# Kernel tuning notes

Measured on AMD Instinct MI355X. Metric: run time of the kernel, lower is better.

Reference implementation:

```python
import jax, jax.numpy as jnp
import numpy as np
import math

NEG_INF = -10000.0

def setup_inputs() -> dict:
    key = jax.random.key(0)
    k1, k2, k3 = jax.random.split(key, 3)
    B, Sq, Sk, H, D = 2, 2048, 2048, 16, 64
    q = jax.random.normal(k1, (B, Sq, H, D), dtype=jnp.float32)
    kv = jax.random.normal(k2, (B, Sk, 2, H, D), dtype=jnp.float32)
    key_padding_mask = jax.random.randint(k3, (B, Sk), 0, 2).astype(jnp.bool_)
    return {"q": q, "kv": kv, "key_padding_mask": key_padding_mask}

def reference(q, kv, key_padding_mask):
    # q: (B, Sq, H, D); kv: (B, Sk, 2, H, D); key_padding_mask: (B, Sk) True=keep
    D = q.shape[-1]
    softmax_scale = 1.0 / math.sqrt(D)
    k = kv[:, :, 0]  # (B, Sk, H, D)
    v = kv[:, :, 1]  # (B, Sk, H, D)
    # (B, H, Sq, Sk) score matrix
    scores = jnp.einsum('bthd,bshd->bhts', q, k * softmax_scale)
    # additive padding mask: 0 where keep, NEG_INF where masked out
    pad = jnp.where(key_padding_mask, 0.0, NEG_INF).astype(scores.dtype)
    scores = scores + pad[:, None, None, :]
    attention = jax.nn.softmax(scores, axis=-1)
    # dropout_p = 0.0 (eval mode) -> no-op
    output = jnp.einsum('bhts,bshd->bthd', attention, v)
    return output
```

## Files before the change

kernel.cpp:

```cpp
#include <hip/hip_runtime.h>

typedef unsigned short u16;
typedef unsigned int   u32;
typedef u16   u16x8 __attribute__((ext_vector_type(8)));
typedef float f32x4 __attribute__((ext_vector_type(4)));
typedef __bf16 bf16x8 __attribute__((ext_vector_type(8)));
typedef u32   u32x2 __attribute__((ext_vector_type(2)));
typedef u32   u32x4 __attribute__((ext_vector_type(4)));

#define QSCALE  0.18033688011112f
#define BM_OPEN  -28.8539008177793f
#define BM_MASK  -14455.8043097f

__device__ __forceinline__ u16 f2bf(float x){
  __bf16 h = (__bf16)x;
  return __builtin_bit_cast(u16, h);
}
__device__ __forceinline__ f32x4 mfma16x16x32(u16x8 a, u16x8 b, f32x4 c){
  return __builtin_amdgcn_mfma_f32_16x16x32_bf16(
      __builtin_bit_cast(bf16x8, a), __builtin_bit_cast(bf16x8, b), c, 0, 0, 0);
}
__device__ __forceinline__ void gld16(const void* g, void* l){
  __builtin_amdgcn_global_load_lds(
      (const __attribute__((address_space(1))) u32*)g,
      (__attribute__((address_space(3))) u32*)l, 16, 0, 0);
}


__global__ __launch_bounds__(256, 4)
void prepass(const float* __restrict__ KV, const int* __restrict__ MASK,
             u16* __restrict__ IMG, float* __restrict__ BIASM)
{
  const int tid = threadIdx.x;
  const int bid = blockIdx.x;
  const int kt = bid & 31;
  const int h  = (bid >> 5) & 15;
  const int b  = bid >> 9;
  const int kb = kt*64;
  const size_t kv_b = (size_t)b*(2048u*2048u);
  u16* tile = IMG + (size_t)bid * 8192;

  {
    const int skey = tid >> 2, scp = tid & 3;
    const float* kp = KV + kv_b + (size_t)(kb + skey)*2048 + h*64 + 16*scp;
    f32x4 f0 = *(const f32x4*)(kp);
    f32x4 f1 = *(const f32x4*)(kp + 4);
    f32x4 f2 = *(const f32x4*)(kp + 8);
    f32x4 f3 = *(const f32x4*)(kp + 12);
    u16x8 c0, c1;
    #pragma unroll
    for (int e = 0; e < 4; ++e){
      c0[e] = f2bf(f0[e]); c0[e+4] = f2bf(f1[e]);
      c1[e] = f2bf(f2[e]); c1[e+4] = f2bf(f3[e]);
    }
    const int idx0 = skey*64 + (((2*scp) ^ (skey & 7)) << 3);
    *(u16x8*)&tile[idx0]     = c0;
    *(u16x8*)&tile[idx0 ^ 8] = c1;
  }
  {
    const int sdb = tid & 7, ssp = tid >> 3;
    const float* vp = KV + kv_b + (size_t)(kb + 2*ssp)*2048 + 1024 + h*64 + 8*sdb;
    f32x4 r0a = *(const f32x4*)(vp);
    f32x4 r0b = *(const f32x4*)(vp + 4);
    f32x4 r1a = *(const f32x4*)(vp + 2048);
    f32x4 r1b = *(const f32x4*)(vp + 2048 + 4);
    u32* vimg = (u32*)(tile + 4096);
    const int wc = ssp >> 2, wi = ssp & 3;
    #pragma unroll
    for (int j = 0; j < 4; ++j){
      const int d0 = 8*sdb + j;
      const int d1 = d0 + 4;
      vimg[d0*32 + ((wc ^ (d0 & 7)) << 2) + wi] = (u32)f2bf(r0a[j]) | ((u32)f2bf(r1a[j]) << 16);
      vimg[d1*32 + ((wc ^ (d1 & 7)) << 2) + wi] = (u32)f2bf(r0b[j]) | ((u32)f2bf(r1b[j]) << 16);
    }
  }
  if (h == 0 && tid < 64){
    const int s = kb + tid;
    BIASM[b*2048 + s] = MASK[b*2048 + s] ? BM_OPEN : BM_MASK;
  }
}

template<int PRE>
__global__ __launch_bounds__(256, 2)
void attn_main(const float* __restrict__ Q, const float* __restrict__ KV,
               const int* __restrict__ MASK, const u16* __restrict__ IMG,
               const float* __restrict__ BIASM, float* __restrict__ OUT)
{
  __shared__ __align__(16) u16 KVbuf[3][8192];
  __shared__ __align__(16) u32 Pw[4][32*36];

  const int tid  = threadIdx.x;
  const int w    = tid >> 6;
  const int lane = tid & 63;
  const int lg   = lane >> 4;
  const int ln   = lane & 15;

  const int bid0 = blockIdx.x;
  const int bid  = (bid0 & 7)*64 + (bid0 >> 3);
  const int qt  = bid & 15;
  const int h   = (bid >> 4) & 15;
  const int b   = bid >> 8;

  const int qbase = qt*128 + w*32;
  const size_t q_b  = (size_t)b * (2048u*1024u);
  const size_t kv_b = (size_t)b * (2048u*2048u);

  const int lnoff = ln*64;
  const int ck0   = ((lg ^ (ln & 7)) << 3);
  const int ck1   = ck0 ^ 32;

  u16x8 Qf[2][2];
  #pragma unroll
  for (int G = 0; G < 2; ++G){
    const int qrow = qbase + 16*G + ln;
    const float* qp = Q + q_b + (size_t)qrow*1024 + h*64 + 8*lg;
    #pragma unroll
    for (int kc = 0; kc < 2; ++kc){
      f32x4 a = *(const f32x4*)(qp + 32*kc);
      f32x4 c = *(const f32x4*)(qp + 32*kc + 4);
      u16x8 v;
      #pragma unroll
      for (int e = 0; e < 4; ++e){
        v[e]     = f2bf(a[e] * QSCALE);
        v[e + 4] = f2bf(c[e] * QSCALE);
      }
      Qf[G][kc] = v;
    }
  }

  f32x4 Oacc[2][4];
  #pragma unroll
  for (int G = 0; G < 2; ++G)
    #pragma unroll
    for (int dt = 0; dt < 4; ++dt)
      Oacc[G][dt] = f32x4{0.f,0.f,0.f,0.f};
  float lrun[2] = { 0.f, 0.f };

  const char* img0 = (const char*)IMG + (size_t)((b*16 + h)*32) * 16384;
  const int so = tid*16;
  const int skey = tid >> 2, scp = tid & 3;
  const int sdb  = tid & 7,  ssp = tid >> 3;
  const float* kp0 = KV + kv_b + (size_t)skey*2048 + h*64 + 16*scp;
  const float* vp0 = KV + kv_b + (size_t)(2*ssp)*2048 + 1024 + h*64 + 8*sdb;
  f32x4 kf0, kf1, kf2, kf3, va, vb2, vc, vd;

#define STAGE_ISSUE(T, DST) do{                                               \
    const char* g_ = img0 + (size_t)(T)*16384;                                \
    char* l_ = (char*)(DST);                                                  \
    gld16(g_+so,        l_+so);                                               \
    gld16(g_+so+4096,   l_+so+4096);                                          \
    gld16(g_+so+8192,   l_+so+8192);                                          \
    gld16(g_+so+12288,  l_+so+12288);                                         \
  }while(0)

#define STAGE_REG(T) do{                                                      \
    const float* kp_ = kp0 + (size_t)(T)*64*2048;                             \
    kf0=*(const f32x4*)(kp_);   kf1=*(const f32x4*)(kp_+4);                   \
    kf2=*(const f32x4*)(kp_+8); kf3=*(const f32x4*)(kp_+12);                  \
    const float* vp_ = vp0 + (size_t)(T)*64*2048;                             \
    va=*(const f32x4*)(vp_);      vb2=*(const f32x4*)(vp_+4);                 \
    vc=*(const f32x4*)(vp_+2048); vd =*(const f32x4*)(vp_+2048+4);            \
  }while(0)

#define STAGE_WRITE(DST) do{                                                  \
    u16x8 c0_, c1_;                                                           \
    _Pragma("unroll") for (int e_=0; e_<4; ++e_){                             \
      c0_[e_]=f2bf(kf0[e_]); c0_[e_+4]=f2bf(kf1[e_]);                         \
      c1_[e_]=f2bf(kf2[e_]); c1_[e_+4]=f2bf(kf3[e_]); }                       \
    const int kix_ = skey*64 + (((2*scp) ^ (skey & 7)) << 3);                 \
    *(u16x8*)&(DST)[kix_]     = c0_;                                          \
    *(u16x8*)&(DST)[kix_ ^ 8] = c1_;                                          \
    u32* vimg_ = (u32*)((DST)+4096);                                          \
    const int wc_ = ssp >> 2, wi_ = ssp & 3;                                  \
    _Pragma("unroll") for (int j_=0; j_<4; ++j_){                             \
      const int d0_=8*sdb+j_, d1_=d0_+4;                                      \
      vimg_[d0_*32 + ((wc_ ^ (d0_&7)) << 2) + wi_] = (u32)f2bf(va[j_])  | ((u32)f2bf(vc[j_])<<16); \
      vimg_[d1_*32 + ((wc_ ^ (d1_&7)) << 2) + wi_] = (u32)f2bf(vb2[j_]) | ((u32)f2bf(vd[j_])<<16); \
    }                                                                         \
  }while(0)

#define COMPUTE(T, CUR) do{                                                   \
    const u16* Kb_ = (CUR);                                                   \
    const u16* Vb_ = (CUR) + 4096;                                            \
    f32x4 S[2][4];                                                            \
    _Pragma("unroll") for (int ct = 0; ct < 4; ++ct){                         \
      f32x4 bv;                                                               \
      if constexpr (PRE){                                                     \
        bv = *(const f32x4*)(BIASM + b*2048 + (T)*64 + 16*ct + 4*lg);         \
      } else {                                                                \
        const int4 mv = *(const int4*)(MASK + b*2048 + (T)*64 + 16*ct + 4*lg);\
        bv[0] = mv.x ? BM_OPEN : BM_MASK;                                     \
        bv[1] = mv.y ? BM_OPEN : BM_MASK;                                     \
        bv[2] = mv.z ? BM_OPEN : BM_MASK;                                     \
        bv[3] = mv.w ? BM_OPEN : BM_MASK;                                     \
      }                                                                       \
      S[0][ct] = bv;                                                          \
      S[1][ct] = bv;                                                          \
    }                                                                         \
    __builtin_amdgcn_s_setprio(1);                                            \
    _Pragma("unroll") for (int ct = 0; ct < 4; ++ct){                         \
      const int rb = ct*1024 + lnoff;                                         \
      u16x8 k0 = *(const u16x8*)&Kb_[rb + ck0];                               \
      u16x8 k1 = *(const u16x8*)&Kb_[rb + ck1];                               \
      S[0][ct] = mfma16x16x32(k0, Qf[0][0], S[0][ct]);                        \
      S[1][ct] = mfma16x16x32(k0, Qf[1][0], S[1][ct]);                        \
      S[0][ct] = mfma16x16x32(k1, Qf[0][1], S[0][ct]);                        \
      S[1][ct] = mfma16x16x32(k1, Qf[1][1], S[1][ct]);                        \
    }                                                                         \
    __builtin_amdgcn_s_setprio(0);                                            \
    _Pragma("unroll") for (int G = 0; G < 2; ++G){                            \
      float ps = 0.f;                                                         \
      _Pragma("unroll") for (int ct = 0; ct < 4; ++ct){                       \
        _Pragma("unroll") for (int r = 0; r < 4; ++r){                        \
          const float p = __builtin_amdgcn_exp2f(S[G][ct][r]);                \
          S[G][ct][r] = p;                                                    \
          ps += p;                                                            \
        }                                                                     \
      }                                                                       \
      lrun[G] += ps;                                                          \
      _Pragma("unroll") for (int ct = 0; ct < 4; ++ct){                       \
        u32x2 pw;                                                             \
        pw[0] = (u32)f2bf(S[G][ct][0]) | ((u32)f2bf(S[G][ct][1]) << 16);      \
        pw[1] = (u32)f2bf(S[G][ct][2]) | ((u32)f2bf(S[G][ct][3]) << 16);      \
        *(u32x2*)&Pw[w][(16*G + ln)*36 + 8*ct + 2*lg] = pw;                   \
      }                                                                       \
    }                                                                         \
    asm volatile("" ::: "memory");                                            \
    u16x8 Pf[2][2];                                                           \
    _Pragma("unroll") for (int G = 0; G < 2; ++G)                             \
      _Pragma("unroll") for (int sc = 0; sc < 2; ++sc){                       \
        u32x4 pr = *(const u32x4*)&Pw[w][(16*G + ln)*36 + 4*lg + 16*sc];      \
        Pf[G][sc] = __builtin_bit_cast(u16x8, pr);                            \
      }                                                                       \
    __builtin_amdgcn_s_setprio(1);                                            \
    _Pragma("unroll") for (int dt = 0; dt < 4; ++dt){                         \
      const int rb = dt*1024 + lnoff;                                         \
      u16x8 v0 = *(const u16x8*)&Vb_[rb + ck0];                               \
      u16x8 v1 = *(const u16x8*)&Vb_[rb + ck1];                               \
      Oacc[0][dt] = mfma16x16x32(v0, Pf[0][0], Oacc[0][dt]);                  \
      Oacc[1][dt] = mfma16x16x32(v0, Pf[1][0], Oacc[1][dt]);                  \
      Oacc[0][dt] = mfma16x16x32(v1, Pf[0][1], Oacc[0][dt]);                  \
      Oacc[1][dt] = mfma16x16x32(v1, Pf[1][1], Oacc[1][dt]);                  \
    }                                                                         \
    __builtin_amdgcn_s_setprio(0);                                            \
  }while(0)

#define SEAM(N) do{                                                           \
    __builtin_amdgcn_sched_barrier(0);                                        \
    asm volatile("s_waitcnt vmcnt(%0)" :: "i"(N) : "memory");                 \
    __builtin_amdgcn_sched_barrier(0);                                        \
    __builtin_amdgcn_s_barrier();                                             \
  }while(0)

#define PITER(T, CUR, FREE) do{                                               \
    if ((T) + 2 <= 31) STAGE_ISSUE((T)+2, FREE);                              \
    COMPUTE(T, CUR);                                                          \
    SEAM(4);                                                                  \
  }while(0)

  if constexpr (PRE){
    u16* b0 = &KVbuf[0][0];
    u16* b1 = &KVbuf[1][0];
    u16* b2 = &KVbuf[2][0];
    STAGE_ISSUE(0, b0);
    STAGE_ISSUE(1, b1);
    SEAM(4);
    for (int u = 0; u < 10; ++u){
      PITER(3*u    , b0, b2);
      PITER(3*u + 1, b1, b0);
      PITER(3*u + 2, b2, b1);
    }
    COMPUTE(30, b0);
    SEAM(0);
    COMPUTE(31, b1);
  } else {
    STAGE_REG(0);
    STAGE_WRITE(&KVbuf[0][0]);
    __syncthreads();
    for (int t = 0; t < 32; ++t){
      if (t < 31) STAGE_REG(t+1);
      COMPUTE(t, &KVbuf[t & 1][0]);
      if (t < 31){
        STAGE_WRITE(&KVbuf[(t+1) & 1][0]);
        __syncthreads();
      }
    }
  }

  #pragma unroll
  for (int G = 0; G < 2; ++G){
    float l_ = lrun[G];
    l_ += __shfl_xor(l_, 16, 64);
    l_ += __shfl_xor(l_, 32, 64);
    const float inv = 1.f / l_;
    const int qrow = qbase + 16*G + ln;
    float* op = OUT + q_b + (size_t)qrow*1024 + h*64;
    #pragma unroll
    for (int dt = 0; dt < 4; ++dt){
      f32x4 ov;
      ov[0] = Oacc[G][dt][0] * inv;
      ov[1] = Oacc[G][dt][1] * inv;
      ov[2] = Oacc[G][dt][2] * inv;
      ov[3] = Oacc[G][dt][3] * inv;
      *(f32x4*)(op + 16*dt + 4*lg) = ov;
    }
  }
#undef STAGE_ISSUE
#undef STAGE_REG
#undef STAGE_WRITE
#undef COMPUTE
#undef SEAM
#undef PITER
}

extern "C" void kernel_launch(void* const* d_in, const int* in_sizes, int n_in,
                              void* d_out, int out_size, void* d_ws, size_t ws_size,
                              hipStream_t stream)
{
  const float* Q  = nullptr;
  const float* KV = nullptr;
  const int*   M  = nullptr;
  for (int i = 0; i < n_in; ++i){
    if      (in_sizes[i] == 4194304) Q  = (const float*)d_in[i];
    else if (in_sizes[i] == 8388608) KV = (const float*)d_in[i];
    else if (in_sizes[i] == 4096)    M  = (const int*)d_in[i];
  }
  if (!Q)  Q  = (const float*)d_in[0];
  if (!KV) KV = (const float*)d_in[1];
  if (!M)  M  = (const int*)d_in[2];
  float* O = (float*)d_out;

  const size_t NEED = 16384ull + 1024ull*16384ull;
  if (ws_size >= NEED){
    float* biasm = (float*)d_ws;
    u16*   img   = (u16*)((char*)d_ws + 16384);
    prepass<<<dim3(1024), dim3(256), 0, stream>>>(KV, M, img, biasm);
    attn_main<1><<<dim3(512), dim3(256), 0, stream>>>(Q, KV, M, img, biasm, O);
  } else {
    attn_main<0><<<dim3(512), dim3(256), 0, stream>>>(Q, KV, M, nullptr, nullptr, O);
  }
}
```

Baseline: 68.15 us.

## Use 8 waves of 16 query rows each instead of 4 waves of 32

Doubles the block to 512 threads so each wave owns 16 query rows instead of 32. This halves per-wave register state (Q fragments, output accumulators, scores) and spreads the staging loads across twice as many threads. It also moves the mask bias from the MFMA accumulator initialisation into the exp2 argument. Each K/V tile is still shared by all 128 rows of a block, but per-wave MFMA work per tile is halved while LDS K/V reads per wave stay the same. That lowers MFMA-to-LDS-read intensity and could make the kernel LDS-bound.

```diff
diff --git a/kernel.cpp b/kernel.cpp
--- a/kernel.cpp
+++ b/kernel.cpp
@@ -81,18 +81,18 @@
 }
 
 template<int PRE>
-__global__ __launch_bounds__(256, 2)
+__global__ __launch_bounds__(512, 4)
 void attn_main(const float* __restrict__ Q, const float* __restrict__ KV,
                const int* __restrict__ MASK, const u16* __restrict__ IMG,
                const float* __restrict__ BIASM, float* __restrict__ OUT)
 {
   __shared__ __align__(16) u16 KVbuf[3][8192];
-  __shared__ __align__(16) u32 Pw[4][32*36];
+  __shared__ __align__(16) u32 Pw[8][16*36];
 
   const int tid  = threadIdx.x;
   const int w    = tid >> 6;
   const int lane = tid & 63;
-  const int lg   = lane >> 4;
+  const int lg   = (lane >> 4) & 3;
   const int ln   = lane & 15;
 
   const int bid0 = blockIdx.x;
@@ -101,7 +101,7 @@
   const int h   = (bid >> 4) & 15;
   const int b   = bid >> 8;
 
-  const int qbase = qt*128 + w*32;
+  const int qbase = qt*128 + w*16;
   const size_t q_b  = (size_t)b * (2048u*1024u);
   const size_t kv_b = (size_t)b * (2048u*2048u);
 
@@ -109,10 +109,9 @@
   const int ck0   = ((lg ^ (ln & 7)) << 3);
   const int ck1   = ck0 ^ 32;
 
-  u16x8 Qf[2][2];
-  #pragma unroll
-  for (int G = 0; G < 2; ++G){
-    const int qrow = qbase + 16*G + ln;
+  u16x8 Qf[2];
+  {
+    const int qrow = qbase + ln;
     const float* qp = Q + q_b + (size_t)qrow*1024 + h*64 + 8*lg;
     #pragma unroll
     for (int kc = 0; kc < 2; ++kc){
@@ -124,123 +123,106 @@
         v[e]     = f2bf(a[e] * QSCALE);
         v[e + 4] = f2bf(c[e] * QSCALE);
       }
-      Qf[G][kc] = v;
-    }
-  }
-
-  f32x4 Oacc[2][4];
+      Qf[kc] = v;
+    }
+  }
+
+  f32x4 Oacc[4];
   #pragma unroll
-  for (int G = 0; G < 2; ++G)
-    #pragma unroll
-    for (int dt = 0; dt < 4; ++dt)
-      Oacc[G][dt] = f32x4{0.f,0.f,0.f,0.f};
-  float lrun[2] = { 0.f, 0.f };
+  for (int dt = 0; dt < 4; ++dt) Oacc[dt] = f32x4{0.f,0.f,0.f,0.f};
+  float lrun = 0.f;
 
   const char* img0 = (const char*)IMG + (size_t)((b*16 + h)*32) * 16384;
   const int so = tid*16;
-  const int skey = tid >> 2, scp = tid & 3;
-  const int sdb  = tid & 7,  ssp = tid >> 3;
-  const float* kp0 = KV + kv_b + (size_t)skey*2048 + h*64 + 16*scp;
-  const float* vp0 = KV + kv_b + (size_t)(2*ssp)*2048 + 1024 + h*64 + 8*sdb;
-  f32x4 kf0, kf1, kf2, kf3, va, vb2, vc, vd;
+  const int skey = tid >> 3, scp7 = tid & 7;
+  const int sdb = tid & 7, spr = (tid >> 3) & 31, vh = tid >> 8;
+  const float* kp0 = KV + kv_b + (size_t)skey*2048 + h*64 + 8*scp7;
+  const float* vp0 = KV + kv_b + (size_t)(2*spr)*2048 + 1024 + h*64 + 8*sdb + 4*vh;
+  f32x4 kfa, kfb, vfa, vfc;
 
 #define STAGE_ISSUE(T, DST) do{                                               \
     const char* g_ = img0 + (size_t)(T)*16384;                                \
     char* l_ = (char*)(DST);                                                  \
     gld16(g_+so,        l_+so);                                               \
-    gld16(g_+so+4096,   l_+so+4096);                                          \
     gld16(g_+so+8192,   l_+so+8192);                                          \
-    gld16(g_+so+12288,  l_+so+12288);                                         \
   }while(0)
 
 #define STAGE_REG(T) do{                                                      \
     const float* kp_ = kp0 + (size_t)(T)*64*2048;                             \
-    kf0=*(const f32x4*)(kp_);   kf1=*(const f32x4*)(kp_+4);                   \
-    kf2=*(const f32x4*)(kp_+8); kf3=*(const f32x4*)(kp_+12);                  \
+    kfa = *(const f32x4*)(kp_); kfb = *(const f32x4*)(kp_+4);                 \
     const float* vp_ = vp0 + (size_t)(T)*64*2048;                             \
-    va=*(const f32x4*)(vp_);      vb2=*(const f32x4*)(vp_+4);                 \
-    vc=*(const f32x4*)(vp_+2048); vd =*(const f32x4*)(vp_+2048+4);            \
+    vfa = *(const f32x4*)(vp_); vfc = *(const f32x4*)(vp_+2048);              \
   }while(0)
 
 #define STAGE_WRITE(DST) do{                                                  \
-    u16x8 c0_, c1_;                                                           \
+    u16x8 c0_;                                                                \
     _Pragma("unroll") for (int e_=0; e_<4; ++e_){                             \
-      c0_[e_]=f2bf(kf0[e_]); c0_[e_+4]=f2bf(kf1[e_]);                         \
-      c1_[e_]=f2bf(kf2[e_]); c1_[e_+4]=f2bf(kf3[e_]); }                       \
-    const int kix_ = skey*64 + (((2*scp) ^ (skey & 7)) << 3);                 \
-    *(u16x8*)&(DST)[kix_]     = c0_;                                          \
-    *(u16x8*)&(DST)[kix_ ^ 8] = c1_;                                          \
+      c0_[e_] = f2bf(kfa[e_]); c0_[e_+4] = f2bf(kfb[e_]); }                   \
+    *(u16x8*)&(DST)[skey*64 + ((scp7 ^ (skey & 7)) << 3)] = c0_;              \
     u32* vimg_ = (u32*)((DST)+4096);                                          \
-    const int wc_ = ssp >> 2, wi_ = ssp & 3;                                  \
+    const int wc_ = spr >> 2, wi_ = spr & 3;                                  \
     _Pragma("unroll") for (int j_=0; j_<4; ++j_){                             \
-      const int d0_=8*sdb+j_, d1_=d0_+4;                                      \
-      vimg_[d0_*32 + ((wc_ ^ (d0_&7)) << 2) + wi_] = (u32)f2bf(va[j_])  | ((u32)f2bf(vc[j_])<<16); \
-      vimg_[d1_*32 + ((wc_ ^ (d1_&7)) << 2) + wi_] = (u32)f2bf(vb2[j_]) | ((u32)f2bf(vd[j_])<<16); \
+      const int d_ = 8*sdb + 4*vh + j_;                                       \
+      vimg_[d_*32 + ((wc_ ^ (d_&7)) << 2) + wi_] =                            \
+          (u32)f2bf(vfa[j_]) | ((u32)f2bf(vfc[j_]) << 16);                    \
     }                                                                         \
   }while(0)
 
 #define COMPUTE(T, CUR) do{                                                   \
     const u16* Kb_ = (CUR);                                                   \
     const u16* Vb_ = (CUR) + 4096;                                            \
-    f32x4 S[2][4];                                                            \
+    f32x4 bv[4];                                                              \
     _Pragma("unroll") for (int ct = 0; ct < 4; ++ct){                         \
-      f32x4 bv;                                                               \
       if constexpr (PRE){                                                     \
-        bv = *(const f32x4*)(BIASM + b*2048 + (T)*64 + 16*ct + 4*lg);         \
+        bv[ct] = *(const f32x4*)(BIASM + b*2048 + (T)*64 + 16*ct + 4*lg);     \
       } else {                                                                \
         const int4 mv = *(const int4*)(MASK + b*2048 + (T)*64 + 16*ct + 4*lg);\
-        bv[0] = mv.x ? BM_OPEN : BM_MASK;                                     \
-        bv[1] = mv.y ? BM_OPEN : BM_MASK;                                     \
-        bv[2] = mv.z ? BM_OPEN : BM_MASK;                                     \
-        bv[3] = mv.w ? BM_OPEN : BM_MASK;                                     \
+        bv[ct][0] = mv.x ? BM_OPEN : BM_MASK;                                 \
+        bv[ct][1] = mv.y ? BM_OPEN : BM_MASK;                                 \
+        bv[ct][2] = mv.z ? BM_OPEN : BM_MASK;                                 \
+        bv[ct][3] = mv.w ? BM_OPEN : BM_MASK;                                 \
       }                                                                       \
-      S[0][ct] = bv;                                                          \
-      S[1][ct] = bv;                                                          \
-    }                                                                         \
+    }                                                                         \
+    f32x4 S[4];                                                               \
+    _Pragma("unroll") for (int ct = 0; ct < 4; ++ct)                          \
+      S[ct] = f32x4{0.f,0.f,0.f,0.f};                                         \
     __builtin_amdgcn_s_setprio(1);                                            \
     _Pragma("unroll") for (int ct = 0; ct < 4; ++ct){                         \
       const int rb = ct*1024 + lnoff;                                         \
       u16x8 k0 = *(const u16x8*)&Kb_[rb + ck0];                               \
       u16x8 k1 = *(const u16x8*)&Kb_[rb + ck1];                               \
-      S[0][ct] = mfma16x16x32(k0, Qf[0][0], S[0][ct]);                        \
-      S[1][ct] = mfma16x16x32(k0, Qf[1][0], S[1][ct]);                        \
-      S[0][ct] = mfma16x16x32(k1, Qf[0][1], S[0][ct]);                        \
-      S[1][ct] = mfma16x16x32(k1, Qf[1][1], S[1][ct]);                        \
+      S[ct] = mfma16x16x32(k0, Qf[0], S[ct]);                                 \
+      S[ct] = mfma16x16x32(k1, Qf[1], S[ct]);                                 \
     }                                                                         \
     __builtin_amdgcn_s_setprio(0);                                            \
-    _Pragma("unroll") for (int G = 0; G < 2; ++G){                            \
-      float ps = 0.f;                                                         \
-      _Pragma("unroll") for (int ct = 0; ct < 4; ++ct){                       \
-        _Pragma("unroll") for (int r = 0; r < 4; ++r){                        \
-          const float p = __builtin_amdgcn_exp2f(S[G][ct][r]);                \
-          S[G][ct][r] = p;                                                    \
-          ps += p;                                                            \
-        }                                                                     \
+    float ps = 0.f;                                                           \
+    _Pragma("unroll") for (int ct = 0; ct < 4; ++ct){                         \
+      _Pragma("unroll") for (int r = 0; r < 4; ++r){                          \
+        const float p = __builtin_amdgcn_exp2f(S[ct][r] + bv[ct][r]);         \
+        S[ct][r] = p;                                                         \
+        ps += p;                                                              \
       }                                                                       \
-      lrun[G] += ps;                                                          \
-      _Pragma("unroll") for (int ct = 0; ct < 4; ++ct){                       \
-        u32x2 pw;                                                             \
-        pw[0] = (u32)f2bf(S[G][ct][0]) | ((u32)f2bf(S[G][ct][1]) << 16);      \
-        pw[1] = (u32)f2bf(S[G][ct][2]) | ((u32)f2bf(S[G][ct][3]) << 16);      \
-        *(u32x2*)&Pw[w][(16*G + ln)*36 + 8*ct + 2*lg] = pw;                   \
-      }                                                                       \
+    }                                                                         \
+    lrun += ps;                                                               \
+    _Pragma("unroll") for (int ct = 0; ct < 4; ++ct){                         \
+      u32x2 pw;                                                               \
+      pw[0] = (u32)f2bf(S[ct][0]) | ((u32)f2bf(S[ct][1]) << 16);              \
+      pw[1] = (u32)f2bf(S[ct][2]) | ((u32)f2bf(S[ct][3]) << 16);              \
+      *(u32x2*)&Pw[w][ln*36 + 8*ct + 2*lg] = pw;                              \
     }                                                                         \
     asm volatile("" ::: "memory");                                            \
-    u16x8 Pf[2][2];                                                           \
-    _Pragma("unroll") for (int G = 0; G < 2; ++G)                             \
-      _Pragma("unroll") for (int sc = 0; sc < 2; ++sc){                       \
-        u32x4 pr = *(const u32x4*)&Pw[w][(16*G + ln)*36 + 4*lg + 16*sc];      \
-        Pf[G][sc] = __builtin_bit_cast(u16x8, pr);                            \
-      }                                                                       \
+    u16x8 Pf[2];                                                              \
+    _Pragma("unroll") for (int sc = 0; sc < 2; ++sc){                         \
+      u32x4 pr = *(const u32x4*)&Pw[w][ln*36 + 4*lg + 16*sc];                 \
+      Pf[sc] = __builtin_bit_cast(u16x8, pr);                                 \
+    }                                                                         \
     __builtin_amdgcn_s_setprio(1);                                            \
     _Pragma("unroll") for (int dt = 0; dt < 4; ++dt){                         \
       const int rb = dt*1024 + lnoff;                                         \
       u16x8 v0 = *(const u16x8*)&Vb_[rb + ck0];                               \
       u16x8 v1 = *(const u16x8*)&Vb_[rb + ck1];                               \
-      Oacc[0][dt] = mfma16x16x32(v0, Pf[0][0], Oacc[0][dt]);                  \
-      Oacc[1][dt] = mfma16x16x32(v0, Pf[1][0], Oacc[1][dt]);                  \
-      Oacc[0][dt] = mfma16x16x32(v1, Pf[0][1], Oacc[0][dt]);                  \
-      Oacc[1][dt] = mfma16x16x32(v1, Pf[1][1], Oacc[1][dt]);                  \
+      Oacc[dt] = mfma16x16x32(v0, Pf[0], Oacc[dt]);                           \
+      Oacc[dt] = mfma16x16x32(v1, Pf[1], Oacc[dt]);                           \
     }                                                                         \
     __builtin_amdgcn_s_setprio(0);                                            \
   }while(0)
@@ -255,7 +237,7 @@
 #define PITER(T, CUR, FREE) do{                                               \
     if ((T) + 2 <= 31) STAGE_ISSUE((T)+2, FREE);                              \
     COMPUTE(T, CUR);                                                          \
-    SEAM(4);                                                                  \
+    SEAM(2);                                                                  \
   }while(0)
 
   if constexpr (PRE){
@@ -264,7 +246,7 @@
     u16* b2 = &KVbuf[2][0];
     STAGE_ISSUE(0, b0);
     STAGE_ISSUE(1, b1);
-    SEAM(4);
+    SEAM(2);
     for (int u = 0; u < 10; ++u){
       PITER(3*u    , b0, b2);
       PITER(3*u + 1, b1, b0);
@@ -287,21 +269,20 @@
     }
   }
 
-  #pragma unroll
-  for (int G = 0; G < 2; ++G){
-    float l_ = lrun[G];
+  {
+    float l_ = lrun;
     l_ += __shfl_xor(l_, 16, 64);
     l_ += __shfl_xor(l_, 32, 64);
     const float inv = 1.f / l_;
-    const int qrow = qbase + 16*G + ln;
+    const int qrow = qbase + ln;
     float* op = OUT + q_b + (size_t)qrow*1024 + h*64;
     #pragma unroll
     for (int dt = 0; dt < 4; ++dt){
       f32x4 ov;
-      ov[0] = Oacc[G][dt][0] * inv;
-      ov[1] = Oacc[G][dt][1] * inv;
-      ov[2] = Oacc[G][dt][2] * inv;
-      ov[3] = Oacc[G][dt][3] * inv;
+      ov[0] = Oacc[dt][0] * inv;
+      ov[1] = Oacc[dt][1] * inv;
+      ov[2] = Oacc[dt][2] * inv;
+      ov[3] = Oacc[dt][3] * inv;
       *(f32x4*)(op + 16*dt + 4*lg) = ov;
     }
   }
@@ -335,8 +316,8 @@
     float* biasm = (float*)d_ws;
     u16*   img   = (u16*)((char*)d_ws + 16384);
     prepass<<<dim3(1024), dim3(256), 0, stream>>>(KV, M, img, biasm);
-    attn_main<1><<<dim3(512), dim3(256), 0, stream>>>(Q, KV, M, img, biasm, O);
+    attn_main<1><<<dim3(512), dim3(512), 0, stream>>>(Q, KV, M, img, biasm, O);
   } else {
-    attn_main<0><<<dim3(512), dim3(256), 0, stream>>>(Q, KV, M, nullptr, nullptr, O);
-  }
-}
+    attn_main<0><<<dim3(512), dim3(512), 0, stream>>>(Q, KV, M, nullptr, nullptr, O);
+  }
+}
```

After: 69.30 us. No clear change (+1.7%).
